# Kernel optimization log

Hardware: AMD Instinct MI355X
Metric: run time of the kernel (lower is better)

## Reference

```python
import jax, jax.numpy as jnp
import numpy as np

N_NODES = 50000
N_EDGES = 800000
IN_CH = 128
HID = 64   # 2 * out_channels
OUT = 32   # out_channels
SLOPE = 0.2  # PyG GATConv default negative_slope


def _gat_layer(x, W, a_src, a_dst, b, src, dst):
    """Single-head GATConv: proj -> edge attention logits -> segment softmax
    over destination nodes -> scatter-aggregate weighted source messages."""
    n = x.shape[0]
    h = x @ W                                   # [N, C]
    ls = h @ a_src                              # [N] per-node src score
    ld = h @ a_dst                              # [N] per-node dst score
    logits = jax.nn.leaky_relu(ls[src] + ld[dst], negative_slope=SLOPE)  # [E]
    # numerically stable segment softmax grouped by destination node
    lmax = jax.ops.segment_max(logits, dst, num_segments=n)              # [N]
    e = jnp.exp(logits - lmax[dst])                                      # [E]
    denom = jax.ops.segment_sum(e, dst, num_segments=n)                  # [N]
    alpha = e / denom[dst]                                               # [E]
    out = jax.ops.segment_sum(alpha[:, None] * h[src], dst, num_segments=n)
    return out + b


def setup_inputs() -> dict:
    key = jax.random.key(0)
    ks = jax.random.split(key, 10)
    x = jax.random.normal(ks[0], (N_NODES, IN_CH), dtype=jnp.float32)
    edge_index = jax.random.randint(ks[1], (2, N_EDGES), 0, N_NODES, dtype=jnp.int32)
    s1 = 1.0 / np.sqrt(IN_CH)
    s2 = 1.0 / np.sqrt(HID)
    return {
        "x": x,
        "edge_index": edge_index,
        "W1": jax.random.normal(ks[2], (IN_CH, HID), dtype=jnp.float32) * s1,
        "a_src1": jax.random.normal(ks[3], (HID,), dtype=jnp.float32) * s2,
        "a_dst1": jax.random.normal(ks[4], (HID,), dtype=jnp.float32) * s2,
        "b1": jnp.zeros((HID,), dtype=jnp.float32),
        "W2": jax.random.normal(ks[5], (HID, OUT), dtype=jnp.float32) * s2,
        "a_src2": jax.random.normal(ks[6], (OUT,), dtype=jnp.float32) / np.sqrt(OUT),
        "a_dst2": jax.random.normal(ks[7], (OUT,), dtype=jnp.float32) / np.sqrt(OUT),
        "b2": jnp.zeros((OUT,), dtype=jnp.float32),
    }


def reference(x, edge_index, W1, a_src1, a_dst1, b1, W2, a_src2, a_dst2, b2):
    src, dst = edge_index[0], edge_index[1]
    h = jax.nn.relu(_gat_layer(x, W1, a_src1, a_dst1, b1, src, dst))
    return _gat_layer(h, W2, a_src2, a_dst2, b2, src, dst)
```

## Files before the change

### kernel.cpp

```cpp
#include <hip/hip_runtime.h>
#include <hip/hip_fp16.h>


#define N_NODES 50000
#define N_EDGES 800000
#define SLOPE 0.2f
#define NBUCK 196
#define CAP 4608

typedef _Float16 half4 __attribute__((ext_vector_type(4)));

__global__ __launch_bounds__(256) void k_zerobins(int* __restrict__ binctr)
{
    if (threadIdx.x < NBUCK) binctr[threadIdx.x] = 0;
}

__global__ __launch_bounds__(1024) void k_bin(
    const int* __restrict__ src, const int* __restrict__ dst,
    int* __restrict__ binctr, int* __restrict__ stg)
{
    __shared__ int hist[NBUCK];
    __shared__ int gb[NBUCK];
    const int t = threadIdx.x;
    if (t < NBUCK) hist[t] = 0;
    __syncthreads();

    const int base = blockIdx.x * 8192;
    int mp[8], mb[8], mr[8];
    int n = 0;
    #pragma unroll
    for (int k = 0; k < 8; ++k) {
        int e = base + t + k * 1024;
        if (e < N_EDGES) {
            int s = src[e], d = dst[e];
            int b = d >> 8;
            mp[n] = s | ((d & 255) << 16);
            mb[n] = b;
            mr[n] = atomicAdd(&hist[b], 1);
            ++n;
        }
    }
    __syncthreads();
    if (t < NBUCK) gb[t] = atomicAdd(&binctr[t], hist[t]);
    __syncthreads();
    for (int i = 0; i < n; ++i)
        stg[mb[i] * CAP + gb[mb[i]] + mr[i]] = mp[i];
}

__global__ __launch_bounds__(256) void k_btot(
    const int* __restrict__ binctr, int* __restrict__ bucket_base)
{
    __shared__ int tmp[256];
    const int t = threadIdx.x;
    int v = (t < NBUCK) ? binctr[t] : 0;
    tmp[t] = v;
    __syncthreads();
    #pragma unroll
    for (int off = 1; off < 256; off <<= 1) {
        int u = (t >= off) ? tmp[t - off] : 0;
        __syncthreads();
        tmp[t] += u;
        __syncthreads();
    }
    if (t < NBUCK) bucket_base[t] = tmp[t] - v;
}

__global__ __launch_bounds__(1024) void k_sort(
    const int* __restrict__ stg,
    const int* __restrict__ binctr, const int* __restrict__ bucket_base,
    int* __restrict__ row_start, int* __restrict__ csr_src)
{
    __shared__ int cnt[256];
    __shared__ int off[256];
    const int b = blockIdx.x, t = threadIdx.x;
    const int n = binctr[b];
    const int sbase = b * CAP;
    const int obase = bucket_base[b];

    if (t < 256) cnt[t] = 0;
    __syncthreads();

    int mv[5], mk[5], mr[5];
    int c = 0;
    for (int i = t; i < n; i += 1024) {
        int v = stg[sbase + i];
        int k = v >> 16;
        mv[c] = v & 0xFFFF;
        mk[c] = k;
        mr[c] = atomicAdd(&cnt[k], 1);
        ++c;
    }
    __syncthreads();

    if (t < 256) off[t] = cnt[t];
    __syncthreads();
    #pragma unroll
    for (int o = 1; o < 256; o <<= 1) {
        int u = (t < 256 && t >= o) ? off[t - o] : 0;
        __syncthreads();
        if (t < 256) off[t] += u;
        __syncthreads();
    }

    if (t < 256) {
        int node = b * 256 + t;
        if (node < N_NODES) row_start[node] = obase + off[t] - cnt[t];
    }
    if (b == NBUCK - 1 && t == 0) row_start[N_NODES] = N_EDGES;

    for (int i = 0; i < c; ++i)
        csr_src[obase + off[mk[i]] - cnt[mk[i]] + mr[i]] = mv[i];
}

__global__ __launch_bounds__(256) void k_gemm1(
    const float* __restrict__ x, const float* __restrict__ W1,
    const float* __restrict__ a_src, const float* __restrict__ a_dst,
    _Float16* __restrict__ h1h, float* __restrict__ ls, float* __restrict__ ld)
{
    __shared__ float As[64][128];
    __shared__ float Bs[128][64];
    const int tid = threadIdx.x;
    const int m0 = blockIdx.x * 64;

    {
        const float4* Wv = (const float4*)W1;
        float4* Bv = (float4*)&Bs[0][0];
        #pragma unroll
        for (int i = 0; i < 8; ++i) Bv[tid + i * 256] = Wv[tid + i * 256];
    }
    {
        const float4* Xv = (const float4*)x;
        #pragma unroll
        for (int i = 0; i < 8; ++i) {
            int idx = tid + i * 256;
            int r = idx >> 5, kq = idx & 31;
            float4 v = make_float4(0.f, 0.f, 0.f, 0.f);
            if (m0 + r < N_NODES) v = Xv[(size_t)(m0 + r) * 32 + kq];
            ((float4*)&As[r][0])[kq] = v;
        }
    }
    __syncthreads();

    const int tx = tid & 15, ty = tid >> 4;
    const int c0 = tx * 4, r0 = ty * 4;
    float acc[4][4] = {};
    for (int k = 0; k < 128; k += 4) {
        float a_s[4][4];
        #pragma unroll
        for (int i = 0; i < 4; ++i) {
            float4 av = *(const float4*)&As[r0 + i][k];
            a_s[i][0] = av.x; a_s[i][1] = av.y; a_s[i][2] = av.z; a_s[i][3] = av.w;
        }
        #pragma unroll
        for (int kk = 0; kk < 4; ++kk) {
            float4 b = *(const float4*)&Bs[k + kk][c0];
            #pragma unroll
            for (int i = 0; i < 4; ++i) {
                acc[i][0] += a_s[i][kk] * b.x;
                acc[i][1] += a_s[i][kk] * b.y;
                acc[i][2] += a_s[i][kk] * b.z;
                acc[i][3] += a_s[i][kk] * b.w;
            }
        }
    }

    float as4[4], ad4[4];
    #pragma unroll
    for (int j = 0; j < 4; ++j) { as4[j] = a_src[c0 + j]; ad4[j] = a_dst[c0 + j]; }

    #pragma unroll
    for (int i = 0; i < 4; ++i) {
        int row = m0 + r0 + i;
        float pls = acc[i][0]*as4[0] + acc[i][1]*as4[1] + acc[i][2]*as4[2] + acc[i][3]*as4[3];
        float pld = acc[i][0]*ad4[0] + acc[i][1]*ad4[1] + acc[i][2]*ad4[2] + acc[i][3]*ad4[3];
        #pragma unroll
        for (int off = 1; off < 16; off <<= 1) {
            pls += __shfl_xor(pls, off, 64);
            pld += __shfl_xor(pld, off, 64);
        }
        if (row < N_NODES) {
            half4 hv;
            hv.x = (_Float16)acc[i][0]; hv.y = (_Float16)acc[i][1];
            hv.z = (_Float16)acc[i][2]; hv.w = (_Float16)acc[i][3];
            ((half4*)&h1h[(size_t)row * 64])[tx] = hv;
            if (tx == 0) { ls[row] = pls; ld[row] = pld; }
        }
    }
}

__global__ __launch_bounds__(256) void k_agg1(
    const int* __restrict__ csr_src, const int* __restrict__ row_start,
    const float* __restrict__ ls, const float* __restrict__ ld,
    const _Float16* __restrict__ h1h, const float* __restrict__ b1,
    float* __restrict__ acc1)
{
    const int node = blockIdx.x * 4 + (threadIdx.x >> 6);
    const int lane = threadIdx.x & 63;
    const int c4 = lane & 15, eslot = lane >> 4;
    const int beg = row_start[node], end = row_start[node + 1];
    const float ldv = ld[node];
    const half4* H = (const half4*)h1h;

    float4 acc = make_float4(0.f, 0.f, 0.f, 0.f);
    float sw = 0.f;
    for (int base = beg; base < end; base += 64) {
        const int cnt = min(64, end - base);
        int s = 0;
        float w = 0.f;
        if (lane < cnt) {
            s = csr_src[base + lane];
            float l = ls[s] + ldv;
            l = l > 0.f ? l : SLOPE * l;
            w = __expf(l);
        }
        float wsum = w;
        #pragma unroll
        for (int off = 1; off < 64; off <<= 1) wsum += __shfl_xor(wsum, off, 64);
        sw += wsum;

        int j = 0;
        for (; j + 8 <= cnt; j += 8) {
            int   s0 = __shfl(s, j + eslot, 64);
            int   s1 = __shfl(s, j + 4 + eslot, 64);
            float w0 = __shfl(w, j + eslot, 64);
            float w1 = __shfl(w, j + 4 + eslot, 64);
            half4 g0 = H[(size_t)s0 * 16 + c4];
            half4 g1 = H[(size_t)s1 * 16 + c4];
            acc.x += w0 * (float)g0.x; acc.y += w0 * (float)g0.y;
            acc.z += w0 * (float)g0.z; acc.w += w0 * (float)g0.w;
            acc.x += w1 * (float)g1.x; acc.y += w1 * (float)g1.y;
            acc.z += w1 * (float)g1.z; acc.w += w1 * (float)g1.w;
        }
        for (; j < cnt; j += 4) {
            int   sj = __shfl(s, j + eslot, 64);
            float wj = __shfl(w, j + eslot, 64);
            half4 g = H[(size_t)sj * 16 + c4];
            acc.x += wj * (float)g.x; acc.y += wj * (float)g.y;
            acc.z += wj * (float)g.z; acc.w += wj * (float)g.w;
        }
    }
    #pragma unroll
    for (int off = 16; off < 64; off <<= 1) {
        acc.x += __shfl_xor(acc.x, off, 64);
        acc.y += __shfl_xor(acc.y, off, 64);
        acc.z += __shfl_xor(acc.z, off, 64);
        acc.w += __shfl_xor(acc.w, off, 64);
    }
    if (eslot == 0) {
        float inv = sw > 0.f ? 1.f / sw : 0.f;
        float4 bb = ((const float4*)b1)[c4];
        ((float4*)&acc1[(size_t)node * 64])[c4] =
            make_float4(acc.x * inv + bb.x, acc.y * inv + bb.y,
                        acc.z * inv + bb.z, acc.w * inv + bb.w);
    }
}

__global__ __launch_bounds__(256) void k_epi1(
    const float* __restrict__ acc1, const float* __restrict__ W2,
    const float* __restrict__ a_src2, const float* __restrict__ a_dst2,
    _Float16* __restrict__ h2h, float* __restrict__ ls2, float* __restrict__ ld2)
{
    __shared__ float Hs[64][68];
    __shared__ float W2s[64][32];
    const int tid = threadIdx.x;
    const int n0 = blockIdx.x * 64;

    {
        const float4* Wv = (const float4*)W2;
        float4* Ws = (float4*)&W2s[0][0];
        Ws[tid] = Wv[tid];
        Ws[tid + 256] = Wv[tid + 256];
    }
    {
        const float4* Av = (const float4*)acc1;
        #pragma unroll
        for (int i = 0; i < 4; ++i) {
            int idx = tid + i * 256;
            int r = idx >> 4, kq = idx & 15;
            float4 v = make_float4(0.f, 0.f, 0.f, 0.f);
            if (n0 + r < N_NODES) {
                v = Av[(size_t)(n0 + r) * 16 + kq];
                v.x = fmaxf(v.x, 0.f); v.y = fmaxf(v.y, 0.f);
                v.z = fmaxf(v.z, 0.f); v.w = fmaxf(v.w, 0.f);
            }
            ((float4*)&Hs[r][0])[kq] = v;
        }
    }
    __syncthreads();

    const int nl = tid >> 2, cg = tid & 3, c0 = cg * 8;
    float acc[8] = {};
    for (int k4 = 0; k4 < 16; ++k4) {
        float4 hv4 = *(const float4*)&Hs[nl][k4 * 4];
        #pragma unroll
        for (int kk = 0; kk < 4; ++kk) {
            float hv = kk == 0 ? hv4.x : kk == 1 ? hv4.y : kk == 2 ? hv4.z : hv4.w;
            int k = k4 * 4 + kk;
            float4 w0 = *(const float4*)&W2s[k][c0];
            float4 w1 = *(const float4*)&W2s[k][c0 + 4];
            acc[0] += hv * w0.x; acc[1] += hv * w0.y;
            acc[2] += hv * w0.z; acc[3] += hv * w0.w;
            acc[4] += hv * w1.x; acc[5] += hv * w1.y;
            acc[6] += hv * w1.z; acc[7] += hv * w1.w;
        }
    }

    float pls = 0.f, pld = 0.f;
    #pragma unroll
    for (int j = 0; j < 8; ++j) {
        pls += acc[j] * a_src2[c0 + j];
        pld += acc[j] * a_dst2[c0 + j];
    }
    pls += __shfl_xor(pls, 1, 64); pls += __shfl_xor(pls, 2, 64);
    pld += __shfl_xor(pld, 1, 64); pld += __shfl_xor(pld, 2, 64);

    int node = n0 + nl;
    if (node < N_NODES) {
        half4 lo, hi;
        lo.x = (_Float16)acc[0]; lo.y = (_Float16)acc[1];
        lo.z = (_Float16)acc[2]; lo.w = (_Float16)acc[3];
        hi.x = (_Float16)acc[4]; hi.y = (_Float16)acc[5];
        hi.z = (_Float16)acc[6]; hi.w = (_Float16)acc[7];
        ((half4*)&h2h[(size_t)node * 32])[cg * 2]     = lo;
        ((half4*)&h2h[(size_t)node * 32])[cg * 2 + 1] = hi;
        if (cg == 0) { ls2[node] = pls; ld2[node] = pld; }
    }
}

__global__ __launch_bounds__(256) void k_agg2(
    const int* __restrict__ csr_src, const int* __restrict__ row_start,
    const float* __restrict__ ls, const float* __restrict__ ld,
    const _Float16* __restrict__ h2h, const float* __restrict__ b2,
    float* __restrict__ out)
{
    const int idx = blockIdx.x * 256 + threadIdx.x;
    const int node = idx >> 5;
    const int grp = idx & 31;
    const int c4 = grp & 7, eslot = grp >> 3;
    const int beg = row_start[node], end = row_start[node + 1];
    const float ldv = ld[node];
    const half4* H = (const half4*)h2h;

    float4 acc = make_float4(0.f, 0.f, 0.f, 0.f);
    float sw = 0.f;
    for (int base = beg; base < end; base += 32) {
        const int cnt = min(32, end - base);
        int s = 0;
        float w = 0.f;
        if (grp < cnt) {
            s = csr_src[base + grp];
            float l = ls[s] + ldv;
            l = l > 0.f ? l : SLOPE * l;
            w = __expf(l);
        }
        float wsum = w;
        #pragma unroll
        for (int off = 1; off < 32; off <<= 1) wsum += __shfl_xor(wsum, off, 32);
        sw += wsum;

        int j = 0;
        for (; j + 8 <= cnt; j += 8) {
            int   s0 = __shfl(s, j + eslot, 32);
            int   s1 = __shfl(s, j + 4 + eslot, 32);
            float w0 = __shfl(w, j + eslot, 32);
            float w1 = __shfl(w, j + 4 + eslot, 32);
            half4 g0 = H[(size_t)s0 * 8 + c4];
            half4 g1 = H[(size_t)s1 * 8 + c4];
            acc.x += w0 * (float)g0.x; acc.y += w0 * (float)g0.y;
            acc.z += w0 * (float)g0.z; acc.w += w0 * (float)g0.w;
            acc.x += w1 * (float)g1.x; acc.y += w1 * (float)g1.y;
            acc.z += w1 * (float)g1.z; acc.w += w1 * (float)g1.w;
        }
        for (; j < cnt; j += 4) {
            int   sj = __shfl(s, j + eslot, 32);
            float wj = __shfl(w, j + eslot, 32);
            half4 g = H[(size_t)sj * 8 + c4];
            acc.x += wj * (float)g.x; acc.y += wj * (float)g.y;
            acc.z += wj * (float)g.z; acc.w += wj * (float)g.w;
        }
    }
    #pragma unroll
    for (int off = 8; off < 32; off <<= 1) {
        acc.x += __shfl_xor(acc.x, off, 32);
        acc.y += __shfl_xor(acc.y, off, 32);
        acc.z += __shfl_xor(acc.z, off, 32);
        acc.w += __shfl_xor(acc.w, off, 32);
    }
    if (eslot == 0) {
        float inv = sw > 0.f ? 1.f / sw : 0.f;
        float4 bb = ((const float4*)b2)[c4];
        ((float4*)&out[(size_t)node * 32])[c4] =
            make_float4(acc.x * inv + bb.x, acc.y * inv + bb.y,
                        acc.z * inv + bb.z, acc.w * inv + bb.w);
    }
}

extern "C" void kernel_launch(void* const* d_in, const int* in_sizes, int n_in,
                              void* d_out, int out_size, void* d_ws, size_t ws_size,
                              hipStream_t stream)
{
    const float* x      = (const float*)d_in[0];
    const int*   ei     = (const int*)  d_in[1];
    const float* W1     = (const float*)d_in[2];
    const float* a_src1 = (const float*)d_in[3];
    const float* a_dst1 = (const float*)d_in[4];
    const float* b1     = (const float*)d_in[5];
    const float* W2     = (const float*)d_in[6];
    const float* a_src2 = (const float*)d_in[7];
    const float* a_dst2 = (const float*)d_in[8];
    const float* b2     = (const float*)d_in[9];
    const int* src = ei;
    const int* dst = ei + N_EDGES;
    float* out = (float*)d_out;

    float* ws   = (float*)d_ws;
    _Float16* h1h = (_Float16*)ws;
    float* acc1 = ws + 1600000;
    float* ls1  = ws + 4800000;
    float* ld1  = ws + 4850000;
    int* row_start   = (int*)(ws + 4900000);
    int* csr_src     = (int*)(ws + 4950016);
    int* binctr      = (int*)(ws + 5750016);
    int* bucket_base = (int*)(ws + 5750272);
    int* stg = (int*)ws;
    _Float16* h2h = h1h;
    float* ls2 = ls1;
    float* ld2 = ld1;

    k_zerobins<<<1,   256,  0, stream>>>(binctr);
    k_bin     <<<98,  1024, 0, stream>>>(src, dst, binctr, stg);
    k_btot    <<<1,   256,  0, stream>>>(binctr, bucket_base);
    k_sort    <<<NBUCK, 1024, 0, stream>>>(stg, binctr, bucket_base,
                                           row_start, csr_src);

    k_gemm1<<<782,   256, 0, stream>>>(x, W1, a_src1, a_dst1, h1h, ls1, ld1);
    k_agg1 <<<12500, 256, 0, stream>>>(csr_src, row_start, ls1, ld1, h1h, b1, acc1);

    k_epi1 <<<782,  256, 0, stream>>>(acc1, W2, a_src2, a_dst2, h2h, ls2, ld2);
    k_agg2 <<<6250, 256, 0, stream>>>(csr_src, row_start, ls2, ld2, h2h, b2, out);
}
```

Measured before the change: 181.5 us.

## Fuse layer-1 aggregation with layer-2 projection and shrink binning blocks

Merges the layer-1 aggregation kernel with the epilogue that applies ReLU, multiplies by W2 and computes the layer-2 attention scores. The 64-wide intermediate no longer makes a float32 round trip through global memory, and one launch is removed. The cost is that every aggregation block now loads W2 into shared memory and runs an extra barrier plus a small per-node matvec. The binning kernel also moves from 98 blocks of 1024 threads to 782 blocks of 256 threads for more parallelism, at the price of more global atomics on the bin counters. The workspace layout is rearranged so h2h and ls2/ld2 no longer alias layer-1 buffers.

```diff
diff --git a/kernel.cpp b/kernel.cpp
--- a/kernel.cpp
+++ b/kernel.cpp
@@ -15,7 +15,7 @@
     if (threadIdx.x < NBUCK) binctr[threadIdx.x] = 0;
 }
 
-__global__ __launch_bounds__(1024) void k_bin(
+__global__ __launch_bounds__(256) void k_bin(
     const int* __restrict__ src, const int* __restrict__ dst,
     int* __restrict__ binctr, int* __restrict__ stg)
 {
@@ -25,12 +25,12 @@
     if (t < NBUCK) hist[t] = 0;
     __syncthreads();
 
-    const int base = blockIdx.x * 8192;
-    int mp[8], mb[8], mr[8];
+    const int base = blockIdx.x * 1024;
+    int mp[4], mb[4], mr[4];
     int n = 0;
     #pragma unroll
-    for (int k = 0; k < 8; ++k) {
-        int e = base + t + k * 1024;
+    for (int k = 0; k < 4; ++k) {
+        int e = base + t + k * 256;
         if (e < N_EDGES) {
             int s = src[e], d = dst[e];
             int b = d >> 8;
@@ -188,14 +188,28 @@
     }
 }
 
-__global__ __launch_bounds__(256) void k_agg1(
+__global__ __launch_bounds__(256) void k_agg1f(
     const int* __restrict__ csr_src, const int* __restrict__ row_start,
     const float* __restrict__ ls, const float* __restrict__ ld,
     const _Float16* __restrict__ h1h, const float* __restrict__ b1,
-    float* __restrict__ acc1)
-{
-    const int node = blockIdx.x * 4 + (threadIdx.x >> 6);
-    const int lane = threadIdx.x & 63;
+    const float* __restrict__ W2,
+    const float* __restrict__ a_src2, const float* __restrict__ a_dst2,
+    _Float16* __restrict__ h2h, float* __restrict__ ls2, float* __restrict__ ld2)
+{
+    __shared__ float W2s[64][32];
+    __shared__ float rows[4][64];
+    const int tid = threadIdx.x;
+    {
+        const float4* Wv = (const float4*)W2;
+        float4* Ws = (float4*)&W2s[0][0];
+        Ws[tid] = Wv[tid];
+        Ws[tid + 256] = Wv[tid + 256];
+    }
+    __syncthreads();
+
+    const int wid = tid >> 6;
+    const int node = blockIdx.x * 4 + wid;
+    const int lane = tid & 63;
     const int c4 = lane & 15, eslot = lane >> 4;
     const int beg = row_start[node], end = row_start[node + 1];
     const float ldv = ld[node];
@@ -249,82 +263,33 @@
     if (eslot == 0) {
         float inv = sw > 0.f ? 1.f / sw : 0.f;
         float4 bb = ((const float4*)b1)[c4];
-        ((float4*)&acc1[(size_t)node * 64])[c4] =
-            make_float4(acc.x * inv + bb.x, acc.y * inv + bb.y,
-                        acc.z * inv + bb.z, acc.w * inv + bb.w);
-    }
-}
-
-__global__ __launch_bounds__(256) void k_epi1(
-    const float* __restrict__ acc1, const float* __restrict__ W2,
-    const float* __restrict__ a_src2, const float* __restrict__ a_dst2,
-    _Float16* __restrict__ h2h, float* __restrict__ ls2, float* __restrict__ ld2)
-{
-    __shared__ float Hs[64][68];
-    __shared__ float W2s[64][32];
-    const int tid = threadIdx.x;
-    const int n0 = blockIdx.x * 64;
-
-    {
-        const float4* Wv = (const float4*)W2;
-        float4* Ws = (float4*)&W2s[0][0];
-        Ws[tid] = Wv[tid];
-        Ws[tid + 256] = Wv[tid + 256];
-    }
-    {
-        const float4* Av = (const float4*)acc1;
-        #pragma unroll
-        for (int i = 0; i < 4; ++i) {
-            int idx = tid + i * 256;
-            int r = idx >> 4, kq = idx & 15;
-            float4 v = make_float4(0.f, 0.f, 0.f, 0.f);
-            if (n0 + r < N_NODES) {
-                v = Av[(size_t)(n0 + r) * 16 + kq];
-                v.x = fmaxf(v.x, 0.f); v.y = fmaxf(v.y, 0.f);
-                v.z = fmaxf(v.z, 0.f); v.w = fmaxf(v.w, 0.f);
-            }
-            ((float4*)&Hs[r][0])[kq] = v;
-        }
-    }
-    __syncthreads();
-
-    const int nl = tid >> 2, cg = tid & 3, c0 = cg * 8;
-    float acc[8] = {};
-    for (int k4 = 0; k4 < 16; ++k4) {
-        float4 hv4 = *(const float4*)&Hs[nl][k4 * 4];
-        #pragma unroll
-        for (int kk = 0; kk < 4; ++kk) {
-            float hv = kk == 0 ? hv4.x : kk == 1 ? hv4.y : kk == 2 ? hv4.z : hv4.w;
-            int k = k4 * 4 + kk;
-            float4 w0 = *(const float4*)&W2s[k][c0];
-            float4 w1 = *(const float4*)&W2s[k][c0 + 4];
-            acc[0] += hv * w0.x; acc[1] += hv * w0.y;
-            acc[2] += hv * w0.z; acc[3] += hv * w0.w;
-            acc[4] += hv * w1.x; acc[5] += hv * w1.y;
-            acc[6] += hv * w1.z; acc[7] += hv * w1.w;
-        }
-    }
-
-    float pls = 0.f, pld = 0.f;
-    #pragma unroll
-    for (int j = 0; j < 8; ++j) {
-        pls += acc[j] * a_src2[c0 + j];
-        pld += acc[j] * a_dst2[c0 + j];
-    }
-    pls += __shfl_xor(pls, 1, 64); pls += __shfl_xor(pls, 2, 64);
-    pld += __shfl_xor(pld, 1, 64); pld += __shfl_xor(pld, 2, 64);
-
-    int node = n0 + nl;
-    if (node < N_NODES) {
-        half4 lo, hi;
-        lo.x = (_Float16)acc[0]; lo.y = (_Float16)acc[1];
-        lo.z = (_Float16)acc[2]; lo.w = (_Float16)acc[3];
-        hi.x = (_Float16)acc[4]; hi.y = (_Float16)acc[5];
-        hi.z = (_Float16)acc[6]; hi.w = (_Float16)acc[7];
-        ((half4*)&h2h[(size_t)node * 32])[cg * 2]     = lo;
-        ((half4*)&h2h[(size_t)node * 32])[cg * 2 + 1] = hi;
-        if (cg == 0) { ls2[node] = pls; ld2[node] = pld; }
-    }
+        float4 r;
+        r.x = fmaxf(acc.x * inv + bb.x, 0.f);
+        r.y = fmaxf(acc.y * inv + bb.y, 0.f);
+        r.z = fmaxf(acc.z * inv + bb.z, 0.f);
+        r.w = fmaxf(acc.w * inv + bb.w, 0.f);
+        ((float4*)&rows[wid][0])[c4] = r;
+    }
+    __syncthreads();
+
+    const int ch = lane & 31;
+    const int kh = (lane >> 5) * 32;
+    const float* row = &rows[wid][0];
+    float hv = 0.f;
+    #pragma unroll
+    for (int k = 0; k < 32; ++k)
+        hv += row[kh + k] * W2s[kh + k][ch];
+    hv += __shfl_xor(hv, 32, 64);
+
+    float pls = hv * a_src2[ch];
+    float pld = hv * a_dst2[ch];
+    #pragma unroll
+    for (int off = 1; off < 32; off <<= 1) {
+        pls += __shfl_xor(pls, off, 64);
+        pld += __shfl_xor(pld, off, 64);
+    }
+    if (lane < 32) h2h[(size_t)node * 32 + ch] = (_Float16)hv;
+    if (lane == 0) { ls2[node] = pls; ld2[node] = pld; }
 }
 
 __global__ __launch_bounds__(256) void k_agg2(
@@ -415,27 +380,25 @@
 
     float* ws   = (float*)d_ws;
     _Float16* h1h = (_Float16*)ws;
-    float* acc1 = ws + 1600000;
-    float* ls1  = ws + 4800000;
-    float* ld1  = ws + 4850000;
-    int* row_start   = (int*)(ws + 4900000);
-    int* csr_src     = (int*)(ws + 4950016);
-    int* binctr      = (int*)(ws + 5750016);
-    int* bucket_base = (int*)(ws + 5750272);
+    _Float16* h2h = (_Float16*)(ws + 1600000);
+    float* ls1  = ws + 2400000;
+    float* ld1  = ws + 2450000;
+    float* ls2  = ws + 2500000;
+    float* ld2  = ws + 2550000;
+    int* row_start   = (int*)(ws + 2600000);
+    int* csr_src     = (int*)(ws + 2650016);
+    int* binctr      = (int*)(ws + 3450016);
+    int* bucket_base = (int*)(ws + 3450272);
     int* stg = (int*)ws;
-    _Float16* h2h = h1h;
-    float* ls2 = ls1;
-    float* ld2 = ld1;
 
     k_zerobins<<<1,   256,  0, stream>>>(binctr);
-    k_bin     <<<98,  1024, 0, stream>>>(src, dst, binctr, stg);
+    k_bin     <<<782, 256,  0, stream>>>(src, dst, binctr, stg);
     k_btot    <<<1,   256,  0, stream>>>(binctr, bucket_base);
     k_sort    <<<NBUCK, 1024, 0, stream>>>(stg, binctr, bucket_base,
                                            row_start, csr_src);
 
     k_gemm1<<<782,   256, 0, stream>>>(x, W1, a_src1, a_dst1, h1h, ls1, ld1);
-    k_agg1 <<<12500, 256, 0, stream>>>(csr_src, row_start, ls1, ld1, h1h, b1, acc1);
-
-    k_epi1 <<<782,  256, 0, stream>>>(acc1, W2, a_src2, a_dst2, h2h, ls2, ld2);
-    k_agg2 <<<6250, 256, 0, stream>>>(csr_src, row_start, ls2, ld2, h2h, b2, out);
-}
+    k_agg1f<<<12500, 256, 0, stream>>>(csr_src, row_start, ls1, ld1, h1h, b1,
+                                       W2, a_src2, a_dst2, h2h, ls2, ld2);
+    k_agg2 <<<6250,  256, 0, stream>>>(csr_src, row_start, ls2, ld2, h2h, b2, out);
+}
```

New measurement: 193.0 us. +6.3%, slower.
